# Optimization experiments

Hardware: AMD Instinct MI355X
Metric: run time of the kernel (lower is better)

## Reference

```python
import jax, jax.numpy as jnp
import numpy as np

N = 100000   # num_entities
R = 8        # num_relations
B = 8        # num_bases = min(R, 30)
D = 128      # hidden_dim == embedding_dim
E = 800000   # num_edges


def rgcn_layer(x, edge_index, edge_type, basis, comp, root, bias):
    """PyG-style RGCNConv with basis decomposition and per-relation mean aggregation.

    Mean aggregation is linear, so we aggregate raw source features per
    (dst, relation) segment first, then apply the relation transform once
    per (node, relation) instead of per edge.
    """
    n, r = x.shape[0], comp.shape[0]
    W = jnp.einsum('rb,bio->rio', comp, basis)          # [R, D_in, D_out]
    src, dst = edge_index[0], edge_index[1]
    seg = dst * r + edge_type                            # segment key per edge
    agg = jax.ops.segment_sum(x[src], seg, num_segments=n * r)          # [N*R, D_in]
    cnt = jax.ops.segment_sum(jnp.ones((src.shape[0],), x.dtype), seg,
                              num_segments=n * r)                        # [N*R]
    agg = (agg / jnp.maximum(cnt, 1.0)[:, None]).reshape(n, r, -1)       # [N, R, D_in]
    return jnp.einsum('nri,rio->no', agg, W) + x @ root + bias


def setup_inputs() -> dict:
    key = jax.random.key(0)
    ks = jax.random.split(key, 12)
    s_in = 1.0 / np.sqrt(D)
    inp = {
        'edge_index': jax.random.randint(ks[0], (2, E), 0, N, dtype=jnp.int64 if jax.config.jax_enable_x64 else jnp.int32),
        'edge_type': jax.random.randint(ks[1], (E,), 0, R, dtype=jnp.int64 if jax.config.jax_enable_x64 else jnp.int32),
        'emb': jax.random.normal(ks[2], (N, D), jnp.float32) * s_in,
        'basis1': jax.random.normal(ks[3], (B, D, D), jnp.float32) * s_in,
        'comp1': jax.random.normal(ks[4], (R, B), jnp.float32) * (1.0 / np.sqrt(B)),
        'root1': jax.random.normal(ks[5], (D, D), jnp.float32) * s_in,
        'bias1': jnp.zeros((D,), jnp.float32),
        'basis2': jax.random.normal(ks[6], (B, D, D), jnp.float32) * s_in,
        'comp2': jax.random.normal(ks[7], (R, B), jnp.float32) * (1.0 / np.sqrt(B)),
        'root2': jax.random.normal(ks[8], (D, D), jnp.float32) * s_in,
        'bias2': jnp.zeros((D,), jnp.float32),
    }
    return inp


def reference(edge_index, edge_type, emb, basis1, comp1, root1, bias1,
              basis2, comp2, root2, bias2):
    # layer 1 + ReLU (dropout is identity at eval time)
    x = rgcn_layer(emb, edge_index, edge_type, basis1, comp1, root1, bias1)
    x = jax.nn.relu(x)
    # layer 2 (output layer, no activation)
    x = rgcn_layer(x, edge_index, edge_type, basis2, comp2, root2, bias2)
    return x
```

## Files before the change

### kernel.cpp

```cpp
#include <hip/hip_runtime.h>

#define NN 100000
#define RR 8
#define BB 8
#define DD 128
#define EE 800000
#define KT 1152
#define NBLK 782
#define NSEG2 (NBLK * 1024)
#define ASTR 40
#define AESTR 40
#define ECH 192

typedef __attribute__((ext_vector_type(8))) __bf16 bf16x8;
typedef __attribute__((ext_vector_type(4))) float f32x4;
typedef __attribute__((ext_vector_type(4))) unsigned int u32x4;

__device__ __forceinline__ unsigned short f2bf(float f) {
    unsigned u = __float_as_uint(f);
    u += 0x7fffu + ((u >> 16) & 1u);
    return (unsigned short)(u >> 16);
}
__device__ __forceinline__ float bf2f(unsigned short h) {
    return __uint_as_float(((unsigned)h) << 16);
}

__global__ __launch_bounds__(256) void k_cvt(const float* __restrict__ x,
                                             unsigned short* __restrict__ xh) {
    int i = blockIdx.x * 256 + threadIdx.x;
    f32x4 a = ((const f32x4*)x)[2 * i];
    f32x4 b = ((const f32x4*)x)[2 * i + 1];
    u32x4 o;
    o[0] = (unsigned)f2bf(a[0]) | ((unsigned)f2bf(a[1]) << 16);
    o[1] = (unsigned)f2bf(a[2]) | ((unsigned)f2bf(a[3]) << 16);
    o[2] = (unsigned)f2bf(b[0]) | ((unsigned)f2bf(b[1]) << 16);
    o[3] = (unsigned)f2bf(b[2]) | ((unsigned)f2bf(b[3]) << 16);
    ((u32x4*)xh)[i] = o;
}

__global__ __launch_bounds__(256) void k_cnt(const int* __restrict__ ei,
                                             const int* __restrict__ et,
                                             int* __restrict__ cnt) {
    int e = blockIdx.x * 256 + threadIdx.x;
    if (e < EE) {
        int d = ei[EE + e];
        atomicAdd(&cnt[(d >> 7) * 1024 + et[e] * 128 + (d & 127)], 1);
    }
}

__global__ __launch_bounds__(256) void k_scan_local(const int* __restrict__ cnt,
                                                    int* __restrict__ loc,
                                                    int* __restrict__ bsum) {
    __shared__ int tmp[256];
    int t = threadIdx.x, i = blockIdx.x * 256 + t;
    int v = cnt[i];
    tmp[t] = v; __syncthreads();
    int val = v;
#pragma unroll
    for (int d = 1; d < 256; d <<= 1) {
        int a = (t >= d) ? tmp[t - d] : 0;
        __syncthreads();
        val += a; tmp[t] = val;
        __syncthreads();
    }
    loc[i] = val - v;
    if (t == 255) bsum[blockIdx.x] = val;
}

__global__ void k_scan_bsum(const int* __restrict__ bsum, int* __restrict__ boff) {
    __shared__ int tmp[256];
    const int NB = NSEG2 / 256;
    const int CH = 13;
    int t = threadIdx.x;
    int base = t * CH, s = 0;
    for (int j = 0; j < CH; ++j) { int idx = base + j; if (idx < NB) s += bsum[idx]; }
    tmp[t] = s; __syncthreads();
    int val = s;
#pragma unroll
    for (int d = 1; d < 256; d <<= 1) {
        int a = (t >= d) ? tmp[t - d] : 0;
        __syncthreads();
        val += a; tmp[t] = val;
        __syncthreads();
    }
    int run = val - s;
    for (int j = 0; j < CH; ++j) { int idx = base + j; if (idx < NB) { boff[idx] = run; run += bsum[idx]; } }
}

__global__ __launch_bounds__(256) void k_scan_add(int* __restrict__ loc,
                                                  const int* __restrict__ boff) {
    int i = blockIdx.x * 256 + threadIdx.x;
    loc[i] += boff[i >> 8];
}

__global__ __launch_bounds__(256) void k_roff(const int* __restrict__ segoff,
                                              int* __restrict__ roff) {
    int idx = blockIdx.x * 256 + threadIdx.x;
    if (idx < NBLK * 8) roff[idx] = segoff[(idx >> 3) * 1024 + (idx & 7) * 128];
    if (idx == NBLK * 8) roff[idx] = EE;
}

__global__ __launch_bounds__(256) void k_scatter(const int* __restrict__ ei,
                                                 const int* __restrict__ et,
                                                 int* __restrict__ segoff,
                                                 int* __restrict__ spk) {
    int e = blockIdx.x * 256 + threadIdx.x;
    if (e < EE) {
        int d = ei[EE + e];
        int key = (d >> 7) * 1024 + et[e] * 128 + (d & 127);
        int pos = atomicAdd(&segoff[key], 1);
        spk[pos] = ei[e];
    }
}

__global__ __launch_bounds__(256) void k_prepB(const float* __restrict__ root,
                                               const float* __restrict__ comp,
                                               const float* __restrict__ basis,
                                               unsigned short* __restrict__ Bhi,
                                               unsigned short* __restrict__ Blo) {
    int idx = blockIdx.x * 256 + threadIdx.x;
    if (idx >= DD * KT) return;
    int o = idx / KT, k = idx - o * KT;
    float v;
    if (k < DD) {
        v = root[k * DD + o];
    } else {
        int r = (k - DD) >> 7, i = (k - DD) & 127;
        float s = 0.f;
#pragma unroll
        for (int b = 0; b < BB; ++b)
            s += comp[r * BB + b] * basis[((size_t)b * DD + i) * DD + o];
        v = s;
    }
    unsigned short hi = f2bf(v);
    Bhi[idx] = hi;
    Blo[idx] = f2bf(v - bf2f(hi));
}

template <bool WRITE_H1>
__global__ __launch_bounds__(256, 3) void k_gemm(
    const unsigned short* __restrict__ xh,
    const unsigned short* __restrict__ Bhi,
    const unsigned short* __restrict__ Blo,
    const float* __restrict__ bias,
    const int* __restrict__ spk,
    const int* __restrict__ roff,
    const int* __restrict__ segend,
    const int* __restrict__ cnt,
    unsigned short* __restrict__ h1h,
    float* __restrict__ outf)
{
    __shared__ unsigned short As[128 * ASTR];
    __shared__ unsigned short Bhs[128 * ASTR];
    __shared__ unsigned short Bls[128 * ASTR];
    __shared__ unsigned short Ae[ECH * AESTR];
    __shared__ int sbeg[1024];
    __shared__ unsigned short scnt[1024];
    __shared__ int reb[9];

    const int tid = threadIdx.x;
    const int b = blockIdx.x;
    const int M0 = b * 128;

    if (tid < 9) reb[tid] = roff[b * 8 + tid];
#pragma unroll
    for (int p = 0; p < 4; ++p) {
        int i = p * 256 + tid;
        int end = segend[b * 1024 + i];
        int c = cnt[b * 1024 + i];
        sbeg[i] = end - c;
        scnt[i] = (unsigned short)c;
    }

    const int wave = tid >> 6, lane = tid & 63;
    const int quad = lane >> 4, lm = lane & 15;
    const int erow = tid >> 1, half = tid & 1;

    float bv[8];
#pragma unroll
    for (int nt = 0; nt < 8; ++nt) bv[nt] = bias[nt * 16 + lm];

    f32x4 acc[2][8];
#pragma unroll
    for (int a = 0; a < 2; ++a)
#pragma unroll
        for (int n = 0; n < 8; ++n) acc[a][n] = (f32x4){0.f, 0.f, 0.f, 0.f};

    __syncthreads();

    for (int ks = 0; ks < KT / 32; ++ks) {
        const int k0 = ks * 32;

        if (ks < 4) {
            int nidx = M0 + erow; if (nidx > NN - 1) nidx = NN - 1;
            const u32x4* px = (const u32x4*)(xh + (size_t)nidx * DD + k0 + half * 16);
            u32x4 a0 = px[0], a1 = px[1];
            __syncthreads();
            unsigned short* pa = &As[erow * ASTR + half * 16];
            *(u32x4*)pa = a0;
            *(u32x4*)(pa + 8) = a1;
        } else {
            const int r = (ks - 4) >> 2;
            const int i0 = ((ks - 4) & 3) * 32;
            const int rb = reb[r], rend = reb[r + 1];
            const int si = r * 128 + erow;
            const int beg = sbeg[si];
            const int cs = scnt[si];
            const int send_ = beg + cs;

            float v[16];
#pragma unroll
            for (int j = 0; j < 16; ++j) v[j] = 0.f;

            if (rb >= rend) __syncthreads();
            for (int cb0 = rb; cb0 < rend; cb0 += ECH) {
                u32x4 a0 = {}, a1 = {}, a2 = {}, a3 = {};
                const int e = cb0 + tid;
                const bool have = (tid < ECH) && (e < rend);
                if (have) {
                    const int s = spk[e];
                    const u32x4* px = (const u32x4*)(xh + (size_t)s * DD + i0);
                    a0 = px[0]; a1 = px[1]; a2 = px[2]; a3 = px[3];
                }
                __syncthreads();
                if (have) {
                    u32x4* pe = (u32x4*)&Ae[tid * AESTR];
                    pe[0] = a0; pe[1] = a1; pe[2] = a2; pe[3] = a3;
                }
                __syncthreads();
                int lo = beg > cb0 ? beg : cb0;
                int hi2 = send_ < cb0 + ECH ? send_ : cb0 + ECH;
                for (int e2 = lo; e2 < hi2; ++e2) {
                    const unsigned* pe = (const unsigned*)&Ae[(e2 - cb0) * AESTR + half * 16];
#pragma unroll
                    for (int q = 0; q < 8; ++q) {
                        unsigned u = pe[q];
                        v[2 * q]     += __uint_as_float(u << 16);
                        v[2 * q + 1] += __uint_as_float(u & 0xFFFF0000u);
                    }
                }
            }
            const float inv = 1.0f / (float)(cs > 1 ? cs : 1);
            unsigned pk8[8];
#pragma unroll
            for (int j = 0; j < 8; ++j)
                pk8[j] = (unsigned)f2bf(v[2 * j] * inv) | ((unsigned)f2bf(v[2 * j + 1] * inv) << 16);
            unsigned short* pa = &As[erow * ASTR + half * 16];
            *(u32x4*)pa = (u32x4){pk8[0], pk8[1], pk8[2], pk8[3]};
            *(u32x4*)(pa + 8) = (u32x4){pk8[4], pk8[5], pk8[6], pk8[7]};
        }

#pragma unroll
        for (int p = 0; p < 2; ++p) {
            int c2 = p * 256 + tid;
            int o = c2 >> 2, q = c2 & 3;
            int goff = o * KT + k0 + q * 8;
            *(u32x4*)&Bhs[o * ASTR + q * 8] = *(const u32x4*)(Bhi + goff);
            *(u32x4*)&Bls[o * ASTR + q * 8] = *(const u32x4*)(Blo + goff);
        }
        __syncthreads();

        bf16x8 af0 = __builtin_bit_cast(bf16x8, *(const u32x4*)&As[(wave * 32 + lm) * ASTR + quad * 8]);
        bf16x8 af1 = __builtin_bit_cast(bf16x8, *(const u32x4*)&As[(wave * 32 + 16 + lm) * ASTR + quad * 8]);
#pragma unroll
        for (int nt = 0; nt < 8; ++nt) {
            bf16x8 bh = __builtin_bit_cast(bf16x8, *(const u32x4*)&Bhs[(nt * 16 + lm) * ASTR + quad * 8]);
            bf16x8 bl = __builtin_bit_cast(bf16x8, *(const u32x4*)&Bls[(nt * 16 + lm) * ASTR + quad * 8]);
            acc[0][nt] = __builtin_amdgcn_mfma_f32_16x16x32_bf16(af0, bh, acc[0][nt], 0, 0, 0);
            acc[0][nt] = __builtin_amdgcn_mfma_f32_16x16x32_bf16(af0, bl, acc[0][nt], 0, 0, 0);
            acc[1][nt] = __builtin_amdgcn_mfma_f32_16x16x32_bf16(af1, bh, acc[1][nt], 0, 0, 0);
            acc[1][nt] = __builtin_amdgcn_mfma_f32_16x16x32_bf16(af1, bl, acc[1][nt], 0, 0, 0);
        }
    }

#pragma unroll
    for (int mt = 0; mt < 2; ++mt) {
#pragma unroll
        for (int nt = 0; nt < 8; ++nt) {
#pragma unroll
            for (int rg = 0; rg < 4; ++rg) {
                int row = M0 + wave * 32 + mt * 16 + quad * 4 + rg;
                if (row < NN) {
                    int col = nt * 16 + lm;
                    float v = acc[mt][nt][rg] + bv[nt];
                    if (WRITE_H1) h1h[(size_t)row * DD + col] = f2bf(fmaxf(v, 0.f));
                    else          outf[(size_t)row * DD + col] = v;
                }
            }
        }
    }
}


extern "C" void kernel_launch(void* const* d_in, const int* in_sizes, int n_in,
                              void* d_out, int out_size, void* d_ws, size_t ws_size,
                              hipStream_t stream) {
    const int*   ei     = (const int*)d_in[0];
    const int*   et     = (const int*)d_in[1];
    const float* emb    = (const float*)d_in[2];
    const float* basis1 = (const float*)d_in[3];
    const float* comp1  = (const float*)d_in[4];
    const float* root1  = (const float*)d_in[5];
    const float* bias1  = (const float*)d_in[6];
    const float* basis2 = (const float*)d_in[7];
    const float* comp2  = (const float*)d_in[8];
    const float* root2  = (const float*)d_in[9];
    const float* bias2  = (const float*)d_in[10];
    float* out = (float*)d_out;
    (void)in_sizes; (void)n_in; (void)out_size; (void)ws_size;

    char* ws = (char*)d_ws;
    int*            cnt    = (int*)(ws + 0);
    int*            segoff = (int*)(ws + 3203072);
    int*            spk    = (int*)(ws + 6406144);
    int*            bsum   = (int*)(ws + 9606144);
    int*            boff   = (int*)(ws + 9618656);
    int*            roffp  = (int*)(ws + 9631168);
    unsigned short* Bhi1   = (unsigned short*)(ws + 9656320);
    unsigned short* Blo1   = (unsigned short*)(ws + 9951232);
    unsigned short* Bhi2   = (unsigned short*)(ws + 10246144);
    unsigned short* Blo2   = (unsigned short*)(ws + 10541056);
    unsigned short* embh   = (unsigned short*)(ws + 10835968);
    unsigned short* h1h    = (unsigned short*)(ws + 36435968);

    hipMemsetAsync(cnt, 0, (size_t)NSEG2 * 4, stream);

    k_cvt       <<<NN * DD / (256 * 8), 256, 0, stream>>>(emb, embh);
    k_cnt       <<<(EE + 255) / 256, 256, 0, stream>>>(ei, et, cnt);
    k_scan_local<<<NSEG2 / 256, 256, 0, stream>>>(cnt, segoff, bsum);
    k_scan_bsum <<<1, 256, 0, stream>>>(bsum, boff);
    k_scan_add  <<<NSEG2 / 256, 256, 0, stream>>>(segoff, boff);
    k_roff      <<<(NBLK * 8 + 256) / 256, 256, 0, stream>>>(segoff, roffp);
    k_scatter   <<<(EE + 255) / 256, 256, 0, stream>>>(ei, et, segoff, spk);

    k_prepB<<<(DD * KT + 255) / 256, 256, 0, stream>>>(root1, comp1, basis1, Bhi1, Blo1);
    k_prepB<<<(DD * KT + 255) / 256, 256, 0, stream>>>(root2, comp2, basis2, Bhi2, Blo2);

    k_gemm<true> <<<NBLK, 256, 0, stream>>>(embh, Bhi1, Blo1, bias1, spk, roffp, segoff, cnt, h1h, nullptr);
    k_gemm<false><<<NBLK, 256, 0, stream>>>(h1h,  Bhi2, Blo2, bias2, spk, roffp, segoff, cnt, nullptr, out);
}
```

Baseline: 564.8 us.

## Restructure gather-GEMM per relation and fuse small setup kernels

The GEMM kernel now gathers each edge's full 128-wide source row once per relation chunk of 64 edges, with software prefetch of the next chunk. Each node's aggregate is accumulated across the whole feature width in registers and the four k-slices are then consumed by MFMA from a single shared tile. B fragments are read directly from global memory instead of being staged in LDS. The old design reloaded edge rows four times per relation and synchronised on every 32-wide k step, which this removes. Separately, the cnt memset is folded into k_cvt, k_roff is merged into the scan-add kernel, and both layers' prepB run in one launch. The trade-offs are higher register use (64 floats per thread, launch bounds lowered to 2 blocks) and B traffic that now goes uncached through global loads.

```diff
diff --git a/kernel.cpp b/kernel.cpp
--- a/kernel.cpp
+++ b/kernel.cpp
@@ -8,9 +8,7 @@
 #define KT 1152
 #define NBLK 782
 #define NSEG2 (NBLK * 1024)
-#define ASTR 40
-#define AESTR 40
-#define ECH 192
+#define AMS 136
 
 typedef __attribute__((ext_vector_type(8))) __bf16 bf16x8;
 typedef __attribute__((ext_vector_type(4))) float f32x4;
@@ -26,8 +24,10 @@
 }
 
 __global__ __launch_bounds__(256) void k_cvt(const float* __restrict__ x,
-                                             unsigned short* __restrict__ xh) {
+                                             unsigned short* __restrict__ xh,
+                                             int* __restrict__ cnt) {
     int i = blockIdx.x * 256 + threadIdx.x;
+    if (i < NSEG2) cnt[i] = 0;
     f32x4 a = ((const f32x4*)x)[2 * i];
     f32x4 b = ((const f32x4*)x)[2 * i + 1];
     u32x4 o;
@@ -87,17 +87,14 @@
     for (int j = 0; j < CH; ++j) { int idx = base + j; if (idx < NB) { boff[idx] = run; run += bsum[idx]; } }
 }
 
-__global__ __launch_bounds__(256) void k_scan_add(int* __restrict__ loc,
-                                                  const int* __restrict__ boff) {
+__global__ __launch_bounds__(256) void k_scan_addroff(int* __restrict__ loc,
+                                                      const int* __restrict__ boff,
+                                                      int* __restrict__ roff) {
     int i = blockIdx.x * 256 + threadIdx.x;
-    loc[i] += boff[i >> 8];
-}
-
-__global__ __launch_bounds__(256) void k_roff(const int* __restrict__ segoff,
-                                              int* __restrict__ roff) {
-    int idx = blockIdx.x * 256 + threadIdx.x;
-    if (idx < NBLK * 8) roff[idx] = segoff[(idx >> 3) * 1024 + (idx & 7) * 128];
-    if (idx == NBLK * 8) roff[idx] = EE;
+    int v = loc[i] + boff[i >> 8];
+    loc[i] = v;
+    if ((i & 127) == 0) roff[(i >> 10) * 8 + ((i >> 7) & 7)] = v;
+    if (i == 0) roff[NBLK * 8] = EE;
 }
 
 __global__ __launch_bounds__(256) void k_scatter(const int* __restrict__ ei,
@@ -113,11 +110,22 @@
     }
 }
 
-__global__ __launch_bounds__(256) void k_prepB(const float* __restrict__ root,
-                                               const float* __restrict__ comp,
-                                               const float* __restrict__ basis,
-                                               unsigned short* __restrict__ Bhi,
-                                               unsigned short* __restrict__ Blo) {
+__global__ __launch_bounds__(256) void k_prepB(const float* __restrict__ root1,
+                                               const float* __restrict__ comp1,
+                                               const float* __restrict__ basis1,
+                                               const float* __restrict__ root2,
+                                               const float* __restrict__ comp2,
+                                               const float* __restrict__ basis2,
+                                               unsigned short* __restrict__ Bhi1,
+                                               unsigned short* __restrict__ Blo1,
+                                               unsigned short* __restrict__ Bhi2,
+                                               unsigned short* __restrict__ Blo2) {
+    const int layer = blockIdx.y;
+    const float* root  = layer ? root2  : root1;
+    const float* comp  = layer ? comp2  : comp1;
+    const float* basis = layer ? basis2 : basis1;
+    unsigned short* Bhi = layer ? Bhi2 : Bhi1;
+    unsigned short* Blo = layer ? Blo2 : Blo1;
     int idx = blockIdx.x * 256 + threadIdx.x;
     if (idx >= DD * KT) return;
     int o = idx / KT, k = idx - o * KT;
@@ -138,7 +146,7 @@
 }
 
 template <bool WRITE_H1>
-__global__ __launch_bounds__(256, 3) void k_gemm(
+__global__ __launch_bounds__(256, 2) void k_gemm(
     const unsigned short* __restrict__ xh,
     const unsigned short* __restrict__ Bhi,
     const unsigned short* __restrict__ Blo,
@@ -150,12 +158,8 @@
     unsigned short* __restrict__ h1h,
     float* __restrict__ outf)
 {
-    __shared__ unsigned short As[128 * ASTR];
-    __shared__ unsigned short Bhs[128 * ASTR];
-    __shared__ unsigned short Bls[128 * ASTR];
-    __shared__ unsigned short Ae[ECH * AESTR];
-    __shared__ int sbeg[1024];
-    __shared__ unsigned short scnt[1024];
+    __shared__ unsigned short Am[128 * AMS];
+    __shared__ unsigned short Ae[64 * AMS];
     __shared__ int reb[9];
 
     const int tid = threadIdx.x;
@@ -163,18 +167,11 @@
     const int M0 = b * 128;
 
     if (tid < 9) reb[tid] = roff[b * 8 + tid];
-#pragma unroll
-    for (int p = 0; p < 4; ++p) {
-        int i = p * 256 + tid;
-        int end = segend[b * 1024 + i];
-        int c = cnt[b * 1024 + i];
-        sbeg[i] = end - c;
-        scnt[i] = (unsigned short)c;
-    }
 
     const int wave = tid >> 6, lane = tid & 63;
     const int quad = lane >> 4, lm = lane & 15;
-    const int erow = tid >> 1, half = tid & 1;
+    const int node = tid >> 1, hh = tid & 1;
+    const int erow = tid >> 2, eq = tid & 3;
 
     float bv[8];
 #pragma unroll
@@ -186,91 +183,123 @@
 #pragma unroll
         for (int n = 0; n < 8; ++n) acc[a][n] = (f32x4){0.f, 0.f, 0.f, 0.f};
 
+    auto mfma_phase = [&](int kg) {
+#pragma unroll
+        for (int kk = 0; kk < 4; ++kk) {
+            bf16x8 af0 = __builtin_bit_cast(bf16x8,
+                *(const u32x4*)&Am[(wave * 32 + lm) * AMS + kk * 32 + quad * 8]);
+            bf16x8 af1 = __builtin_bit_cast(bf16x8,
+                *(const u32x4*)&Am[(wave * 32 + 16 + lm) * AMS + kk * 32 + quad * 8]);
+            const int kb = kg + kk * 32 + quad * 8;
+#pragma unroll
+            for (int nt = 0; nt < 8; ++nt) {
+                const size_t ro = (size_t)(nt * 16 + lm) * KT + kb;
+                bf16x8 bh = __builtin_bit_cast(bf16x8, *(const u32x4*)(Bhi + ro));
+                bf16x8 bl = __builtin_bit_cast(bf16x8, *(const u32x4*)(Blo + ro));
+                acc[0][nt] = __builtin_amdgcn_mfma_f32_16x16x32_bf16(af0, bh, acc[0][nt], 0, 0, 0);
+                acc[0][nt] = __builtin_amdgcn_mfma_f32_16x16x32_bf16(af0, bl, acc[0][nt], 0, 0, 0);
+                acc[1][nt] = __builtin_amdgcn_mfma_f32_16x16x32_bf16(af1, bh, acc[1][nt], 0, 0, 0);
+                acc[1][nt] = __builtin_amdgcn_mfma_f32_16x16x32_bf16(af1, bl, acc[1][nt], 0, 0, 0);
+            }
+        }
+    };
+
+    {
+        int nidx = M0 + node; if (nidx > NN - 1) nidx = NN - 1;
+        const u32x4* px = (const u32x4*)(xh + (size_t)nidx * DD + hh * 64);
+        u32x4 a0 = px[0], a1 = px[1], a2 = px[2], a3 = px[3];
+        u32x4 a4 = px[4], a5 = px[5], a6 = px[6], a7 = px[7];
+        u32x4* pa = (u32x4*)&Am[node * AMS + hh * 64];
+        pa[0] = a0; pa[1] = a1; pa[2] = a2; pa[3] = a3;
+        pa[4] = a4; pa[5] = a5; pa[6] = a6; pa[7] = a7;
+    }
     __syncthreads();
-
-    for (int ks = 0; ks < KT / 32; ++ks) {
-        const int k0 = ks * 32;
-
-        if (ks < 4) {
-            int nidx = M0 + erow; if (nidx > NN - 1) nidx = NN - 1;
-            const u32x4* px = (const u32x4*)(xh + (size_t)nidx * DD + k0 + half * 16);
-            u32x4 a0 = px[0], a1 = px[1];
+    mfma_phase(0);
+
+    for (int r = 0; r < RR; ++r) {
+        const int rb = reb[r], rend = reb[r + 1];
+        const int g = b * 1024 + r * 128 + node;
+        const int send = segend[g];
+        const int cs = cnt[g];
+        const int beg = send - cs;
+        const int nch = (rend - rb + 63) >> 6;
+
+        float v[64];
+#pragma unroll
+        for (int j = 0; j < 64; ++j) v[j] = 0.f;
+
+        u32x4 p0 = {}, p1 = {}, p2 = {}, p3 = {};
+        {
+            int e = rb + erow;
+            if (e < rend) {
+                int s = spk[e];
+                const u32x4* px = (const u32x4*)(xh + (size_t)s * DD + eq * 32);
+                p0 = px[0]; p1 = px[1]; p2 = px[2]; p3 = px[3];
+            }
+        }
+
+        for (int c = 0; c < nch; ++c) {
+            const int cb0 = rb + c * 64;
             __syncthreads();
-            unsigned short* pa = &As[erow * ASTR + half * 16];
-            *(u32x4*)pa = a0;
-            *(u32x4*)(pa + 8) = a1;
-        } else {
-            const int r = (ks - 4) >> 2;
-            const int i0 = ((ks - 4) & 3) * 32;
-            const int rb = reb[r], rend = reb[r + 1];
-            const int si = r * 128 + erow;
-            const int beg = sbeg[si];
-            const int cs = scnt[si];
-            const int send_ = beg + cs;
-
-            float v[16];
-#pragma unroll
-            for (int j = 0; j < 16; ++j) v[j] = 0.f;
-
-            if (rb >= rend) __syncthreads();
-            for (int cb0 = rb; cb0 < rend; cb0 += ECH) {
-                u32x4 a0 = {}, a1 = {}, a2 = {}, a3 = {};
-                const int e = cb0 + tid;
-                const bool have = (tid < ECH) && (e < rend);
-                if (have) {
-                    const int s = spk[e];
-                    const u32x4* px = (const u32x4*)(xh + (size_t)s * DD + i0);
-                    a0 = px[0]; a1 = px[1]; a2 = px[2]; a3 = px[3];
+            if (cb0 + erow < rend) {
+                u32x4* pa = (u32x4*)&Ae[erow * AMS + eq * 32];
+                pa[0] = p0; pa[1] = p1; pa[2] = p2; pa[3] = p3;
+            }
+            {
+                int e = cb0 + 64 + erow;
+                if (e < rend) {
+                    int s = spk[e];
+                    const u32x4* px = (const u32x4*)(xh + (size_t)s * DD + eq * 32);
+                    p0 = px[0]; p1 = px[1]; p2 = px[2]; p3 = px[3];
                 }
-                __syncthreads();
-                if (have) {
-                    u32x4* pe = (u32x4*)&Ae[tid * AESTR];
-                    pe[0] = a0; pe[1] = a1; pe[2] = a2; pe[3] = a3;
+            }
+            __syncthreads();
+            int lo = beg > cb0 ? beg : cb0;
+            int hi2 = send < cb0 + 64 ? send : cb0 + 64;
+            for (int e2 = lo; e2 < hi2; ++e2) {
+                const int slot = e2 - cb0;
+                const u32x4* pe0 = (const u32x4*)&Ae[slot * AMS + hh * 32];
+                const u32x4* pe1 = (const u32x4*)&Ae[slot * AMS + 64 + hh * 32];
+                u32x4 qa0 = pe0[0], qa1 = pe0[1], qa2 = pe0[2], qa3 = pe0[3];
+                u32x4 qb0 = pe1[0], qb1 = pe1[1], qb2 = pe1[2], qb3 = pe1[3];
+#pragma unroll
+                for (int j = 0; j < 4; ++j) {
+                    unsigned u;
+                    u = qa0[j]; v[2*j]      += __uint_as_float(u << 16); v[2*j+1]    += __uint_as_float(u & 0xFFFF0000u);
+                    u = qa1[j]; v[8+2*j]    += __uint_as_float(u << 16); v[8+2*j+1]  += __uint_as_float(u & 0xFFFF0000u);
+                    u = qa2[j]; v[16+2*j]   += __uint_as_float(u << 16); v[16+2*j+1] += __uint_as_float(u & 0xFFFF0000u);
+                    u = qa3[j]; v[24+2*j]   += __uint_as_float(u << 16); v[24+2*j+1] += __uint_as_float(u & 0xFFFF0000u);
+                    u = qb0[j]; v[32+2*j]   += __uint_as_float(u << 16); v[32+2*j+1] += __uint_as_float(u & 0xFFFF0000u);
+                    u = qb1[j]; v[40+2*j]   += __uint_as_float(u << 16); v[40+2*j+1] += __uint_as_float(u & 0xFFFF0000u);
+                    u = qb2[j]; v[48+2*j]   += __uint_as_float(u << 16); v[48+2*j+1] += __uint_as_float(u & 0xFFFF0000u);
+                    u = qb3[j]; v[56+2*j]   += __uint_as_float(u << 16); v[56+2*j+1] += __uint_as_float(u & 0xFFFF0000u);
                 }
-                __syncthreads();
-                int lo = beg > cb0 ? beg : cb0;
-                int hi2 = send_ < cb0 + ECH ? send_ : cb0 + ECH;
-                for (int e2 = lo; e2 < hi2; ++e2) {
-                    const unsigned* pe = (const unsigned*)&Ae[(e2 - cb0) * AESTR + half * 16];
-#pragma unroll
-                    for (int q = 0; q < 8; ++q) {
-                        unsigned u = pe[q];
-                        v[2 * q]     += __uint_as_float(u << 16);
-                        v[2 * q + 1] += __uint_as_float(u & 0xFFFF0000u);
-                    }
-                }
-            }
-            const float inv = 1.0f / (float)(cs > 1 ? cs : 1);
-            unsigned pk8[8];
-#pragma unroll
-            for (int j = 0; j < 8; ++j)
-                pk8[j] = (unsigned)f2bf(v[2 * j] * inv) | ((unsigned)f2bf(v[2 * j + 1] * inv) << 16);
-            unsigned short* pa = &As[erow * ASTR + half * 16];
-            *(u32x4*)pa = (u32x4){pk8[0], pk8[1], pk8[2], pk8[3]};
-            *(u32x4*)(pa + 8) = (u32x4){pk8[4], pk8[5], pk8[6], pk8[7]};
-        }
-
-#pragma unroll
-        for (int p = 0; p < 2; ++p) {
-            int c2 = p * 256 + tid;
-            int o = c2 >> 2, q = c2 & 3;
-            int goff = o * KT + k0 + q * 8;
-            *(u32x4*)&Bhs[o * ASTR + q * 8] = *(const u32x4*)(Bhi + goff);
-            *(u32x4*)&Bls[o * ASTR + q * 8] = *(const u32x4*)(Blo + goff);
-        }
-        __syncthreads();
-
-        bf16x8 af0 = __builtin_bit_cast(bf16x8, *(const u32x4*)&As[(wave * 32 + lm) * ASTR + quad * 8]);
-        bf16x8 af1 = __builtin_bit_cast(bf16x8, *(const u32x4*)&As[(wave * 32 + 16 + lm) * ASTR + quad * 8]);
-#pragma unroll
-        for (int nt = 0; nt < 8; ++nt) {
-            bf16x8 bh = __builtin_bit_cast(bf16x8, *(const u32x4*)&Bhs[(nt * 16 + lm) * ASTR + quad * 8]);
-            bf16x8 bl = __builtin_bit_cast(bf16x8, *(const u32x4*)&Bls[(nt * 16 + lm) * ASTR + quad * 8]);
-            acc[0][nt] = __builtin_amdgcn_mfma_f32_16x16x32_bf16(af0, bh, acc[0][nt], 0, 0, 0);
-            acc[0][nt] = __builtin_amdgcn_mfma_f32_16x16x32_bf16(af0, bl, acc[0][nt], 0, 0, 0);
-            acc[1][nt] = __builtin_amdgcn_mfma_f32_16x16x32_bf16(af1, bh, acc[1][nt], 0, 0, 0);
-            acc[1][nt] = __builtin_amdgcn_mfma_f32_16x16x32_bf16(af1, bl, acc[1][nt], 0, 0, 0);
-        }
+            }
+        }
+        if (nch == 0) __syncthreads();
+
+        const float inv = 1.0f / (float)(cs > 1 ? cs : 1);
+        {
+            unsigned pk[16];
+#pragma unroll
+            for (int j = 0; j < 16; ++j)
+                pk[j] = (unsigned)f2bf(v[2*j] * inv) | ((unsigned)f2bf(v[2*j+1] * inv) << 16);
+            u32x4* pa = (u32x4*)&Am[node * AMS + hh * 32];
+            pa[0] = (u32x4){pk[0],  pk[1],  pk[2],  pk[3]};
+            pa[1] = (u32x4){pk[4],  pk[5],  pk[6],  pk[7]};
+            pa[2] = (u32x4){pk[8],  pk[9],  pk[10], pk[11]};
+            pa[3] = (u32x4){pk[12], pk[13], pk[14], pk[15]};
+#pragma unroll
+            for (int j = 0; j < 16; ++j)
+                pk[j] = (unsigned)f2bf(v[32+2*j] * inv) | ((unsigned)f2bf(v[32+2*j+1] * inv) << 16);
+            u32x4* pb = (u32x4*)&Am[node * AMS + 64 + hh * 32];
+            pb[0] = (u32x4){pk[0],  pk[1],  pk[2],  pk[3]};
+            pb[1] = (u32x4){pk[4],  pk[5],  pk[6],  pk[7]};
+            pb[2] = (u32x4){pk[8],  pk[9],  pk[10], pk[11]};
+            pb[3] = (u32x4){pk[12], pk[13], pk[14], pk[15]};
+        }
+        __syncthreads();
+        mfma_phase(DD + r * DD);
     }
 
 #pragma unroll
@@ -282,9 +311,9 @@
                 int row = M0 + wave * 32 + mt * 16 + quad * 4 + rg;
                 if (row < NN) {
                     int col = nt * 16 + lm;
-                    float v = acc[mt][nt][rg] + bv[nt];
-                    if (WRITE_H1) h1h[(size_t)row * DD + col] = f2bf(fmaxf(v, 0.f));
-                    else          outf[(size_t)row * DD + col] = v;
+                    float vv = acc[mt][nt][rg] + bv[nt];
+                    if (WRITE_H1) h1h[(size_t)row * DD + col] = f2bf(fmaxf(vv, 0.f));
+                    else          outf[(size_t)row * DD + col] = vv;
                 }
             }
         }
@@ -323,18 +352,16 @@
     unsigned short* embh   = (unsigned short*)(ws + 10835968);
     unsigned short* h1h    = (unsigned short*)(ws + 36435968);
 
-    hipMemsetAsync(cnt, 0, (size_t)NSEG2 * 4, stream);
-
-    k_cvt       <<<NN * DD / (256 * 8), 256, 0, stream>>>(emb, embh);
-    k_cnt       <<<(EE + 255) / 256, 256, 0, stream>>>(ei, et, cnt);
-    k_scan_local<<<NSEG2 / 256, 256, 0, stream>>>(cnt, segoff, bsum);
-    k_scan_bsum <<<1, 256, 0, stream>>>(bsum, boff);
-    k_scan_add  <<<NSEG2 / 256, 256, 0, stream>>>(segoff, boff);
-    k_roff      <<<(NBLK * 8 + 256) / 256, 256, 0, stream>>>(segoff, roffp);
-    k_scatter   <<<(EE + 255) / 256, 256, 0, stream>>>(ei, et, segoff, spk);
-
-    k_prepB<<<(DD * KT + 255) / 256, 256, 0, stream>>>(root1, comp1, basis1, Bhi1, Blo1);
-    k_prepB<<<(DD * KT + 255) / 256, 256, 0, stream>>>(root2, comp2, basis2, Bhi2, Blo2);
+    k_cvt         <<<NN * DD / (256 * 8), 256, 0, stream>>>(emb, embh, cnt);
+    k_cnt         <<<(EE + 255) / 256, 256, 0, stream>>>(ei, et, cnt);
+    k_scan_local  <<<NSEG2 / 256, 256, 0, stream>>>(cnt, segoff, bsum);
+    k_scan_bsum   <<<1, 256, 0, stream>>>(bsum, boff);
+    k_scan_addroff<<<NSEG2 / 256, 256, 0, stream>>>(segoff, boff, roffp);
+    k_scatter     <<<(EE + 255) / 256, 256, 0, stream>>>(ei, et, segoff, spk);
+
+    dim3 pgrid((DD * KT + 255) / 256, 2);
+    k_prepB<<<pgrid, 256, 0, stream>>>(root1, comp1, basis1, root2, comp2, basis2,
+                                       Bhi1, Blo1, Bhi2, Blo2);
 
     k_gemm<true> <<<NBLK, 256, 0, stream>>>(embh, Bhi1, Blo1, bias1, spk, roffp, segoff, cnt, h1h, nullptr);
     k_gemm<false><<<NBLK, 256, 0, stream>>>(h1h,  Bhi2, Blo2, bias2, spk, roffp, segoff, cnt, nullptr, out);
```

After: 834.0 us. +47.7%, slower.
